# Optimization experiments

Measured on AMD Instinct MI355X. Metric: run time of the kernel, lower is better.

## Reference

```python
import jax, jax.numpy as jnp
import numpy as np

H, C = 4, 32  # heads, per-head channels
EPS = 1e-5


def setup_inputs() -> dict:
    key = jax.random.key(0)
    ks = jax.random.split(key, 12)
    N, E, IN = 100000, 1600000, 16
    lut_idx = jnp.arange(1024, dtype=jnp.int32)
    x = jax.random.normal(ks[0], (N, IN), dtype=jnp.float32)
    # LUT flag column: exactly the lut_idx nodes have value 1.0 (matches x[:,15]==1.0 mask)
    x = x.at[:, 15].set(0.0).at[lut_idx, 15].set(1.0)
    edge_index = jax.random.randint(ks[1], (2, E), 0, N, dtype=jnp.int64)
    s = 0.1
    return {
        "x": x,
        "edge_index": edge_index,
        "lut_idx": lut_idx,
        "W_lin": jax.random.normal(ks[2], (IN, H * C), dtype=jnp.float32) * s,
        "att_src": jax.random.normal(ks[3], (H, C), dtype=jnp.float32) * s,
        "att_dst": jax.random.normal(ks[4], (H, C), dtype=jnp.float32) * s,
        "bias_gat": jnp.zeros((H * C,), dtype=jnp.float32),
        "gamma": jnp.ones((H * C,), dtype=jnp.float32),
        "beta": jnp.zeros((H * C,), dtype=jnp.float32),
        "W1": jax.random.normal(ks[5], (H * C, 32), dtype=jnp.float32) * s,
        "b1": jnp.zeros((32,), dtype=jnp.float32),
        "W2": jax.random.normal(ks[6], (32, 1), dtype=jnp.float32) * s,
        "b2": jnp.zeros((1,), dtype=jnp.float32),
    }


def gat_conv(x, edge_index, W_lin, att_src, att_dst, bias_gat):
    N = x.shape[0]
    # add self-loops (PyG GATConv default)
    loops = jnp.arange(N, dtype=edge_index.dtype)
    src = jnp.concatenate([edge_index[0], loops])
    dst = jnp.concatenate([edge_index[1], loops])
    h = (x @ W_lin).reshape(N, H, C)                      # [N,H,C]
    a_src = (h * att_src[None]).sum(-1)                   # [N,H]
    a_dst = (h * att_dst[None]).sum(-1)                   # [N,H]
    e = jax.nn.leaky_relu(a_src[src] + a_dst[dst], 0.2)   # [Etot,H]
    m = jax.ops.segment_max(e, dst, num_segments=N)       # stable softmax per dst
    e = jnp.exp(e - m[dst])
    denom = jax.ops.segment_sum(e, dst, num_segments=N)
    alpha = e / denom[dst]                                # [Etot,H]
    msg = h[src] * alpha[:, :, None]                      # [Etot,H,C]
    out = jax.ops.segment_sum(msg, dst, num_segments=N)   # [N,H,C]
    return out.reshape(N, H * C) + bias_gat


def reference(x, edge_index, lut_idx, W_lin, att_src, att_dst, bias_gat,
              gamma, beta, W1, b1, W2, b2):
    h = gat_conv(x, edge_index, W_lin, att_src, att_dst, bias_gat)
    # BatchNorm over nodes (training-mode batch stats, biased var, eps=1e-5)
    mean = h.mean(axis=0)
    var = h.var(axis=0)
    h = (h - mean) / jnp.sqrt(var + EPS) * gamma + beta
    h = jax.nn.relu(h)
    emb = h[lut_idx]                                      # masked LUT nodes
    z = jax.nn.leaky_relu(emb @ W1 + b1, 0.01)            # Dropout is identity in eval
    out = z @ W2 + b2                                     # [n_lut, 1]
    return jnp.squeeze(out, axis=0) if out.shape[0] == 1 else out
```

## Files before the change

kernel.cpp:

```cpp
#include <hip/hip_runtime.h>
#include <hip/hip_fp16.h>
#include <cstdint>
#include <cstring>

typedef unsigned int uint;

#define BSHIFT 8
#define NBUCK 512
#define TILE 4096
#define SCAT_T 512
#define FUSE_T 1024
#define SORT_CAP 5120

__device__ __forceinline__ float leaky02(float x) { return x > 0.f ? x : 0.2f * x; }
__device__ __forceinline__ float bflo(uint u) { return __uint_as_float(u << 16); }
__device__ __forceinline__ float bfhi(uint u) { return __uint_as_float(u & 0xffff0000u); }

__device__ __forceinline__ uint pack_bf16x2(float a, float b) {
    uint ua = __float_as_uint(a), ub = __float_as_uint(b);
    ua += 0x7fffu + ((ua >> 16) & 1u);
    ub += 0x7fffu + ((ub >> 16) & 1u);
    return (ua >> 16) | (ub & 0xffff0000u);
}

__device__ __forceinline__ uint packh2(float a, float b) {
    __half ha = __float2half_rn(a), hb = __float2half_rn(b);
    unsigned short ua, ub;
    memcpy(&ua, &ha, 2);
    memcpy(&ub, &hb, 2);
    return (uint)ua | ((uint)ub << 16);
}

__device__ __forceinline__ float h2f_sel(uint2 xw, int head) {
    uint wrd = (head & 2) ? xw.y : xw.x;
    unsigned short us = (unsigned short)((head & 1) ? (wrd >> 16) : (wrd & 0xffffu));
    __half hh; memcpy(&hh, &us, 2);
    return __half2float(hh);
}

__global__ void k_linear(const float* __restrict__ x, const float* __restrict__ W,
                         const float* __restrict__ att_s, const float* __restrict__ att_d,
                         uint* __restrict__ h, float* __restrict__ a_src,
                         float* __restrict__ a_dst, int* __restrict__ cursor,
                         float* __restrict__ sums, float* __restrict__ sumsq, int N) {
    int tid = threadIdx.x;
    __shared__ float sx[32][16];
    __shared__ float sWs[64], sWd[64];
    int j = tid & 63;
    int sub = tid >> 6;
    int n0 = blockIdx.x * 32;

    if (blockIdx.x == 0) {
        cursor[tid] = 0; cursor[tid + 256] = 0;
        if (tid < 128) sums[tid] = 0.f;
        else sumsq[tid - 128] = 0.f;
    }

    float2 wreg[16];
#pragma unroll
    for (int k = 0; k < 16; k++) wreg[k] = ((const float2*)(W + k * 128))[j];

    if (tid < 128) {
        int row = tid >> 2;
        if (n0 + row < N)
            ((float4*)sx)[tid] = ((const float4*)(x + (size_t)n0 * 16))[tid];
    } else if (tid < 192) {
        int t = tid - 128;
        int k = t >> 2, hh = t & 3;
        float s1 = 0.f, s2 = 0.f;
        for (int c = 0; c < 32; c++) {
            float wv = W[k * 128 + hh * 32 + c];
            s1 += wv * att_s[hh * 32 + c];
            s2 += wv * att_d[hh * 32 + c];
        }
        sWs[t] = s1;
        sWd[t] = s2;
    }
    __syncthreads();

#pragma unroll
    for (int i = 0; i < 8; i++) {
        int loc = sub + i * 4;
        int n = n0 + loc;
        if (n >= N) break;
        float acc0 = 0.f, acc1 = 0.f;
#pragma unroll
        for (int k = 0; k < 16; k++) {
            float xk = sx[loc][k];
            acc0 += xk * wreg[k].x;
            acc1 += xk * wreg[k].y;
        }
        h[(size_t)n * 64 + j] = pack_bf16x2(acc0, acc1);
    }

    int loc2 = tid >> 3, hh = (tid >> 1) & 3, sd = tid & 1;
    int n2 = n0 + loc2;
    if (n2 < N) {
        const float* Wm = sd ? sWd : sWs;
        float acc = 0.f;
#pragma unroll
        for (int k = 0; k < 16; k++) acc += sx[loc2][k] * Wm[k * 4 + hh];
        if (sd) a_dst[n2 * 4 + hh] = acc;
        else    a_src[n2 * 4 + hh] = acc;
    }
}

__global__ void kb_scatter(const int* __restrict__ src, const int* __restrict__ dst, int E,
                           int* __restrict__ cursor, uint* __restrict__ pairs) {
    __shared__ int tileCnt[NBUCK], tileCnt2[NBUCK], tileOff[NBUCK], gbase[NBUCK];
    __shared__ int wsum[8], wbase[8];
    __shared__ uint lp[TILE];
    __shared__ unsigned short lb[TILE];
    int tid = threadIdx.x;
    int l = tid & 63, w = tid >> 6;
    int t0 = blockIdx.x * TILE;
    tileCnt[tid] = 0;
    tileCnt2[tid] = 0;
    __syncthreads();
    int dreg[8], sreg[8];
#pragma unroll
    for (int j = 0; j < 8; j++) {
        int idx = t0 + j * SCAT_T + tid;
        if (idx < E) {
            dreg[j] = dst[idx];
            sreg[j] = src[idx];
            atomicAdd(&tileCnt[dreg[j] >> BSHIFT], 1);
        } else dreg[j] = -1;
    }
    __syncthreads();
    int v = tileCnt[tid];
    int s = v;
#pragma unroll
    for (int off = 1; off < 64; off <<= 1) {
        int t = __shfl_up(s, off);
        if (l >= off) s += t;
    }
    if (l == 63) wsum[w] = s;
    __syncthreads();
    if (tid < 8) {
        int b = 0;
        for (int i = 0; i < tid; i++) b += wsum[i];
        wbase[tid] = b;
    }
    __syncthreads();
    int ex = s - v + wbase[w];
    tileOff[tid] = ex;
    if (v > 0) gbase[tid] = atomicAdd(&cursor[tid], v);
    __syncthreads();
#pragma unroll
    for (int j = 0; j < 8; j++) {
        if (dreg[j] >= 0) {
            int bk = dreg[j] >> BSHIFT;
            int r = atomicAdd(&tileCnt2[bk], 1);
            int pos = tileOff[bk] + r;
            lp[pos] = ((uint)sreg[j] << BSHIFT) | (uint)(dreg[j] & 255);
            lb[pos] = (unsigned short)bk;
        }
    }
    __syncthreads();
    int tot = min(TILE, E - t0);
    for (int k = tid; k < tot; k += SCAT_T) {
        int bk = lb[k];
        int lpos = gbase[bk] + (k - tileOff[bk]);
        if (lpos < SORT_CAP)
            pairs[(size_t)bk * SORT_CAP + lpos] = lp[k];
    }
}

__global__ void kb_sortgat(const uint* __restrict__ pairs, const int* __restrict__ cursor,
                           const float* __restrict__ a_src, const float* __restrict__ a_dst,
                           const uint* __restrict__ h, const float* __restrict__ bias,
                           uint* __restrict__ hagg, int N) {
    __shared__ int cnt[256], off0[256], degl[256];
    __shared__ int wsum[4], wbase[4];
    __shared__ uint lcode[SORT_CAP];
    __shared__ uint2 wlds[SORT_CAP];
    __shared__ float4 sad[256], sas[256];
    int tid = threadIdx.x;
    int l = tid & 63, w = tid >> 6;
    int b = blockIdx.x;
    int n0 = b << BSHIFT;
    int nn = min(256, N - n0);
    int ebase = b * SORT_CAP;
    int ecnt = cursor[b];
    if (ecnt > SORT_CAP) ecnt = SORT_CAP;
    if (tid < 256) cnt[tid] = 0;
    if (tid < nn) {
        sad[tid] = ((const float4*)a_dst)[n0 + tid];
        sas[tid] = ((const float4*)a_src)[n0 + tid];
    }
    __syncthreads();
    for (int k = tid; k < ecnt; k += FUSE_T)
        atomicAdd(&cnt[pairs[ebase + k] & 255], 1);
    __syncthreads();
    int v = (tid < 256) ? cnt[tid] : 0;
    int s = v;
#pragma unroll
    for (int off = 1; off < 64; off <<= 1) {
        int t = __shfl_up(s, off);
        if (l >= off) s += t;
    }
    if (tid < 256 && l == 63) wsum[w] = s;
    __syncthreads();
    if (tid < 4) {
        int base = 0;
        for (int i = 0; i < tid; i++) base += wsum[i];
        wbase[tid] = base;
    }
    __syncthreads();
    if (tid < 256) {
        off0[tid] = s - v + wbase[w];
        degl[tid] = v;
    }
    __syncthreads();
    if (tid < 256) cnt[tid] = 0;
    __syncthreads();
    for (int k = tid; k < ecnt; k += FUSE_T) {
        uint p = pairs[ebase + k];
        int ln = p & 255;
        int r = atomicAdd(&cnt[ln], 1);
        lcode[off0[ln] + r] = p;
    }
    __syncthreads();
    for (int k = tid; k < ecnt; k += FUSE_T) {
        uint p = lcode[k];
        int src = (int)(p >> BSHIFT);
        int ln = p & 255;
        float4 as = ((const float4*)a_src)[src];
        float4 ad = sad[ln];
        float w0 = __expf(leaky02(as.x + ad.x));
        float w1 = __expf(leaky02(as.y + ad.y));
        float w2 = __expf(leaky02(as.z + ad.z));
        float w3 = __expf(leaky02(as.w + ad.w));
        wlds[k] = make_uint2(packh2(w0, w1), packh2(w2, w3));
    }
    __syncthreads();
    int q = l >> 4;
    int l16 = l & 15;
    int head = l16 >> 2;
    for (int pass = 0; pass < 4; pass++) {
        int ln = pass * 64 + w * 4 + q;
        if (ln >= nn) continue;
        int d = n0 + ln;
        int ebs = off0[ln];
        int deg = degl[ln];
        float asv = ((const float*)sas)[ln * 4 + head];
        float adv = ((const float*)sad)[ln * 4 + head];
        float wslf = __expf(leaky02(asv + adv));
        uint4 u = ((const uint4*)(h + (size_t)d * 64))[l16];
        float sum = wslf;
        float2 a01 = make_float2(wslf * bflo(u.x), wslf * bfhi(u.x));
        float2 a23 = make_float2(wslf * bflo(u.y), wslf * bfhi(u.y));
        float2 a45 = make_float2(wslf * bflo(u.z), wslf * bfhi(u.z));
        float2 a67 = make_float2(wslf * bflo(u.w), wslf * bfhi(u.w));

        int i = 0;
        for (; i + 3 < deg; i += 4) {
            uint p0 = lcode[ebs + i];
            uint p1 = lcode[ebs + i + 1];
            uint p2 = lcode[ebs + i + 2];
            uint p3 = lcode[ebs + i + 3];
            uint2 x0 = wlds[ebs + i];
            uint2 x1 = wlds[ebs + i + 1];
            uint2 x2 = wlds[ebs + i + 2];
            uint2 x3 = wlds[ebs + i + 3];
            float w0 = h2f_sel(x0, head);
            float w1 = h2f_sel(x1, head);
            float w2 = h2f_sel(x2, head);
            float w3 = h2f_sel(x3, head);
            uint4 u0 = ((const uint4*)(h + (size_t)(p0 >> BSHIFT) * 64))[l16];
            uint4 u1 = ((const uint4*)(h + (size_t)(p1 >> BSHIFT) * 64))[l16];
            uint4 u2 = ((const uint4*)(h + (size_t)(p2 >> BSHIFT) * 64))[l16];
            uint4 u3 = ((const uint4*)(h + (size_t)(p3 >> BSHIFT) * 64))[l16];
            sum += (w0 + w1) + (w2 + w3);
            float2 w02 = {w0, w0}, w12 = {w1, w1}, w22 = {w2, w2}, w32 = {w3, w3};
            a01 += make_float2(bflo(u0.x), bfhi(u0.x)) * w02
                 + make_float2(bflo(u1.x), bfhi(u1.x)) * w12
                 + make_float2(bflo(u2.x), bfhi(u2.x)) * w22
                 + make_float2(bflo(u3.x), bfhi(u3.x)) * w32;
            a23 += make_float2(bflo(u0.y), bfhi(u0.y)) * w02
                 + make_float2(bflo(u1.y), bfhi(u1.y)) * w12
                 + make_float2(bflo(u2.y), bfhi(u2.y)) * w22
                 + make_float2(bflo(u3.y), bfhi(u3.y)) * w32;
            a45 += make_float2(bflo(u0.z), bfhi(u0.z)) * w02
                 + make_float2(bflo(u1.z), bfhi(u1.z)) * w12
                 + make_float2(bflo(u2.z), bfhi(u2.z)) * w22
                 + make_float2(bflo(u3.z), bfhi(u3.z)) * w32;
            a67 += make_float2(bflo(u0.w), bfhi(u0.w)) * w02
                 + make_float2(bflo(u1.w), bfhi(u1.w)) * w12
                 + make_float2(bflo(u2.w), bfhi(u2.w)) * w22
                 + make_float2(bflo(u3.w), bfhi(u3.w)) * w32;
        }
        for (; i < deg; i++) {
            uint p0 = lcode[ebs + i];
            float w0 = h2f_sel(wlds[ebs + i], head);
            uint4 u0 = ((const uint4*)(h + (size_t)(p0 >> BSHIFT) * 64))[l16];
            sum += w0;
            float2 w02 = {w0, w0};
            a01 += make_float2(bflo(u0.x), bfhi(u0.x)) * w02;
            a23 += make_float2(bflo(u0.y), bfhi(u0.y)) * w02;
            a45 += make_float2(bflo(u0.z), bfhi(u0.z)) * w02;
            a67 += make_float2(bflo(u0.w), bfhi(u0.w)) * w02;
        }
        float inv = 1.f / sum;
        float4 b0 = ((const float4*)bias)[2 * l16];
        float4 b1 = ((const float4*)bias)[2 * l16 + 1];
        uint4 o;
        o.x = pack_bf16x2(a01.x * inv + b0.x, a01.y * inv + b0.y);
        o.y = pack_bf16x2(a23.x * inv + b0.z, a23.y * inv + b0.w);
        o.z = pack_bf16x2(a45.x * inv + b1.x, a45.y * inv + b1.y);
        o.w = pack_bf16x2(a67.x * inv + b1.z, a67.y * inv + b1.w);
        ((uint4*)(hagg + (size_t)d * 64))[l16] = o;
    }
}

__global__ void k_bnstats(const uint* __restrict__ hagg, int N,
                          float* __restrict__ sums, float* __restrict__ sumsq) {
    int t = threadIdx.x;
    int cg = t & 31, rs = t >> 5;
    float4 s = make_float4(0.f, 0.f, 0.f, 0.f), q = make_float4(0.f, 0.f, 0.f, 0.f);
    for (int n = blockIdx.x * 8 + rs; n < N; n += gridDim.x * 8) {
        uint2 u = ((const uint2*)(hagg + (size_t)n * 64))[cg];
        float v0 = bflo(u.x), v1 = bfhi(u.x), v2 = bflo(u.y), v3 = bfhi(u.y);
        s.x += v0; s.y += v1; s.z += v2; s.w += v3;
        q.x += v0 * v0; q.y += v1 * v1; q.z += v2 * v2; q.w += v3 * v3;
    }
    __shared__ float4 ls[256], lq[256];
    ls[t] = s; lq[t] = q;
    __syncthreads();
    if (t < 32) {
        float4 S = ls[t], Q = lq[t];
        for (int r = 1; r < 8; r++) {
            float4 a = ls[t + r * 32], b = lq[t + r * 32];
            S.x += a.x; S.y += a.y; S.z += a.z; S.w += a.w;
            Q.x += b.x; Q.y += b.y; Q.z += b.z; Q.w += b.w;
        }
        atomicAdd(&sums[t * 4 + 0], S.x);
        atomicAdd(&sums[t * 4 + 1], S.y);
        atomicAdd(&sums[t * 4 + 2], S.z);
        atomicAdd(&sums[t * 4 + 3], S.w);
        atomicAdd(&sumsq[t * 4 + 0], Q.x);
        atomicAdd(&sumsq[t * 4 + 1], Q.y);
        atomicAdd(&sumsq[t * 4 + 2], Q.z);
        atomicAdd(&sumsq[t * 4 + 3], Q.w);
    }
}

__global__ void k_mlp(const uint* __restrict__ hagg, const int* __restrict__ lut,
                      const float* __restrict__ sums, const float* __restrict__ sumsq,
                      const float* __restrict__ gamma, const float* __restrict__ beta,
                      const float* __restrict__ W1, const float* __restrict__ b1,
                      const float* __restrict__ W2, const float* __restrict__ b2,
                      float* __restrict__ out, int N, int nlut) {
    int blk = blockIdx.x;
    if (blk >= nlut) return;
    int node = lut[blk];
    int lane = threadIdx.x;
    __shared__ float v[128];
    float invN = 1.f / (float)N;
    uint u = hagg[(size_t)node * 64 + lane];
    int c0 = 2 * lane, c1 = 2 * lane + 1;
    {
        float mean = sums[c0] * invN;
        float var = sumsq[c0] * invN - mean * mean;
        float val = (bflo(u) - mean) / sqrtf(var + 1e-5f) * gamma[c0] + beta[c0];
        v[c0] = fmaxf(val, 0.f);
        mean = sums[c1] * invN;
        var = sumsq[c1] * invN - mean * mean;
        val = (bfhi(u) - mean) / sqrtf(var + 1e-5f) * gamma[c1] + beta[c1];
        v[c1] = fmaxf(val, 0.f);
    }
    __syncthreads();
    float r = 0.f;
    if (lane < 32) {
        float z = b1[lane];
        for (int c = 0; c < 128; c++) z += v[c] * W1[c * 32 + lane];
        z = z > 0.f ? z : 0.01f * z;
        r = z * W2[lane];
    }
#pragma unroll
    for (int off = 16; off >= 1; off >>= 1) r += __shfl_xor(r, off);
    if (lane == 0) out[blk] = r + b2[0];
}

extern "C" void kernel_launch(void* const* d_in, const int* in_sizes, int n_in,
                              void* d_out, int out_size, void* d_ws, size_t ws_size,
                              hipStream_t stream) {
    const float* x     = (const float*)d_in[0];
    const int*   edges = (const int*)d_in[1];
    const int*   lut   = (const int*)d_in[2];
    const float* W_lin = (const float*)d_in[3];
    const float* att_s = (const float*)d_in[4];
    const float* att_d = (const float*)d_in[5];
    const float* bias  = (const float*)d_in[6];
    const float* gamma = (const float*)d_in[7];
    const float* beta  = (const float*)d_in[8];
    const float* W1    = (const float*)d_in[9];
    const float* b1    = (const float*)d_in[10];
    const float* W2    = (const float*)d_in[11];
    const float* b2    = (const float*)d_in[12];

    int N = in_sizes[0] / 16;
    int E = in_sizes[1] / 2;
    int nlut = in_sizes[2];
    int B = (N + 255) >> BSHIFT;

    const int* esrc = edges;
    const int* edst = edges + E;

    char* ws = (char*)d_ws;
    size_t off = 0;
    auto alloc = [&](size_t bytes) -> void* {
        void* p = ws + off;
        off += (bytes + 255) & ~(size_t)255;
        return p;
    };
    uint*  h       = (uint*)alloc((size_t)N * 64 * 4);
    uint*  hagg    = (uint*)alloc((size_t)N * 64 * 4);
    float* a_src   = (float*)alloc((size_t)N * 4 * 4);
    float* a_dst   = (float*)alloc((size_t)N * 4 * 4);
    uint*  pairs   = (uint*)alloc((size_t)B * SORT_CAP * 4);
    int*   cursor  = (int*)alloc((size_t)NBUCK * 4);
    float* sums    = (float*)alloc(128 * 4);
    float* sumsq   = (float*)alloc(128 * 4);

    k_linear<<<(N + 31) / 32, 256, 0, stream>>>(x, W_lin, att_s, att_d, h,
                                                a_src, a_dst, cursor, sums, sumsq, N);
    kb_scatter<<<(E + TILE - 1) / TILE, SCAT_T, 0, stream>>>(esrc, edst, E, cursor, pairs);
    kb_sortgat<<<B, FUSE_T, 0, stream>>>(pairs, cursor, a_src, a_dst, h, bias, hagg, N);
    k_bnstats<<<256, 256, 0, stream>>>(hagg, N, sums, sumsq);
    k_mlp<<<nlut, 64, 0, stream>>>(hagg, lut, sums, sumsq, gamma, beta, W1, b1, W2, b2,
                                   (float*)d_out, N, nlut);
}
```

Measured before the change: 233.9 us.

## Fuse BatchNorm statistics into GAT aggregation and write only LUT rows

Removes the separate k_bnstats kernel. Per-channel sum and sum-of-squares are now accumulated in registers inside kb_sortgat, reduced with shuffles and LDS, and added to global sums with atomics. Aggregated rows are written to hagg only for LUT nodes, marked by a flag array that k_linear clears and kb_scatter sets. This skips most of the hagg write and the full re-read, at the cost of more per-block atomics and extra reduction work. The counting-sort scatter pass and the attention-weight pass are also merged, lcode now stores raw source indices, and a launch-bounds hint is added.

Result: faster. 211.3 us (-9.7%).

```diff
diff --git a/kernel.cpp b/kernel.cpp
--- a/kernel.cpp
+++ b/kernel.cpp
@@ -42,7 +42,8 @@
                          const float* __restrict__ att_s, const float* __restrict__ att_d,
                          uint* __restrict__ h, float* __restrict__ a_src,
                          float* __restrict__ a_dst, int* __restrict__ cursor,
-                         float* __restrict__ sums, float* __restrict__ sumsq, int N) {
+                         float* __restrict__ sums, float* __restrict__ sumsq,
+                         unsigned char* __restrict__ flags, int N) {
     int tid = threadIdx.x;
     __shared__ float sx[32][16];
     __shared__ float sWs[64], sWd[64];
@@ -55,6 +56,7 @@
         if (tid < 128) sums[tid] = 0.f;
         else sumsq[tid - 128] = 0.f;
     }
+    if (tid < 32 && n0 + tid < N) flags[n0 + tid] = 0;
 
     float2 wreg[16];
 #pragma unroll
@@ -106,7 +108,9 @@
 }
 
 __global__ void kb_scatter(const int* __restrict__ src, const int* __restrict__ dst, int E,
-                           int* __restrict__ cursor, uint* __restrict__ pairs) {
+                           int* __restrict__ cursor, uint* __restrict__ pairs,
+                           const int* __restrict__ lut, int nlut,
+                           unsigned char* __restrict__ flags) {
     __shared__ int tileCnt[NBUCK], tileCnt2[NBUCK], tileOff[NBUCK], gbase[NBUCK];
     __shared__ int wsum[8], wbase[8];
     __shared__ uint lp[TILE];
@@ -114,6 +118,9 @@
     int tid = threadIdx.x;
     int l = tid & 63, w = tid >> 6;
     int t0 = blockIdx.x * TILE;
+    if (blockIdx.x == 0) {
+        for (int k = tid; k < nlut; k += SCAT_T) flags[lut[k]] = 1;
+    }
     tileCnt[tid] = 0;
     tileCnt2[tid] = 0;
     __syncthreads();
@@ -167,15 +174,18 @@
     }
 }
 
-__global__ void kb_sortgat(const uint* __restrict__ pairs, const int* __restrict__ cursor,
+__global__ void __launch_bounds__(1024, 8) kb_sortgat(
+                           const uint* __restrict__ pairs, const int* __restrict__ cursor,
                            const float* __restrict__ a_src, const float* __restrict__ a_dst,
                            const uint* __restrict__ h, const float* __restrict__ bias,
-                           uint* __restrict__ hagg, int N) {
+                           const unsigned char* __restrict__ flags,
+                           uint* __restrict__ hagg,
+                           float* __restrict__ sums, float* __restrict__ sumsq, int N) {
     __shared__ int cnt[256], off0[256], degl[256];
     __shared__ int wsum[4], wbase[4];
     __shared__ uint lcode[SORT_CAP];
     __shared__ uint2 wlds[SORT_CAP];
-    __shared__ float4 sad[256], sas[256];
+    __shared__ float4 sad[256];
     int tid = threadIdx.x;
     int l = tid & 63, w = tid >> 6;
     int b = blockIdx.x;
@@ -185,10 +195,7 @@
     int ecnt = cursor[b];
     if (ecnt > SORT_CAP) ecnt = SORT_CAP;
     if (tid < 256) cnt[tid] = 0;
-    if (tid < nn) {
-        sad[tid] = ((const float4*)a_dst)[n0 + tid];
-        sas[tid] = ((const float4*)a_src)[n0 + tid];
-    }
+    if (tid < nn) sad[tid] = ((const float4*)a_dst)[n0 + tid];
     __syncthreads();
     for (int k = tid; k < ecnt; k += FUSE_T)
         atomicAdd(&cnt[pairs[ebase + k] & 255], 1);
@@ -218,33 +225,32 @@
     for (int k = tid; k < ecnt; k += FUSE_T) {
         uint p = pairs[ebase + k];
         int ln = p & 255;
+        int src = (int)(p >> BSHIFT);
         int r = atomicAdd(&cnt[ln], 1);
-        lcode[off0[ln] + r] = p;
-    }
-    __syncthreads();
-    for (int k = tid; k < ecnt; k += FUSE_T) {
-        uint p = lcode[k];
-        int src = (int)(p >> BSHIFT);
-        int ln = p & 255;
+        int pos = off0[ln] + r;
+        lcode[pos] = (uint)src;
         float4 as = ((const float4*)a_src)[src];
         float4 ad = sad[ln];
-        float w0 = __expf(leaky02(as.x + ad.x));
-        float w1 = __expf(leaky02(as.y + ad.y));
-        float w2 = __expf(leaky02(as.z + ad.z));
-        float w3 = __expf(leaky02(as.w + ad.w));
-        wlds[k] = make_uint2(packh2(w0, w1), packh2(w2, w3));
+        wlds[pos] = make_uint2(
+            packh2(__expf(leaky02(as.x + ad.x)), __expf(leaky02(as.y + ad.y))),
+            packh2(__expf(leaky02(as.z + ad.z)), __expf(leaky02(as.w + ad.w))));
     }
     __syncthreads();
     int q = l >> 4;
     int l16 = l & 15;
     int head = l16 >> 2;
+    float4 b0 = ((const float4*)bias)[2 * l16];
+    float4 b1 = ((const float4*)bias)[2 * l16 + 1];
+    float sv[8], sq[8];
+#pragma unroll
+    for (int j = 0; j < 8; j++) { sv[j] = 0.f; sq[j] = 0.f; }
     for (int pass = 0; pass < 4; pass++) {
         int ln = pass * 64 + w * 4 + q;
         if (ln >= nn) continue;
         int d = n0 + ln;
         int ebs = off0[ln];
         int deg = degl[ln];
-        float asv = ((const float*)sas)[ln * 4 + head];
+        float asv = a_src[d * 4 + head];
         float adv = ((const float*)sad)[ln * 4 + head];
         float wslf = __expf(leaky02(asv + adv));
         uint4 u = ((const uint4*)(h + (size_t)d * 64))[l16];
@@ -268,10 +274,10 @@
             float w1 = h2f_sel(x1, head);
             float w2 = h2f_sel(x2, head);
             float w3 = h2f_sel(x3, head);
-            uint4 u0 = ((const uint4*)(h + (size_t)(p0 >> BSHIFT) * 64))[l16];
-            uint4 u1 = ((const uint4*)(h + (size_t)(p1 >> BSHIFT) * 64))[l16];
-            uint4 u2 = ((const uint4*)(h + (size_t)(p2 >> BSHIFT) * 64))[l16];
-            uint4 u3 = ((const uint4*)(h + (size_t)(p3 >> BSHIFT) * 64))[l16];
+            uint4 u0 = ((const uint4*)(h + (size_t)p0 * 64))[l16];
+            uint4 u1 = ((const uint4*)(h + (size_t)p1 * 64))[l16];
+            uint4 u2 = ((const uint4*)(h + (size_t)p2 * 64))[l16];
+            uint4 u3 = ((const uint4*)(h + (size_t)p3 * 64))[l16];
             sum += (w0 + w1) + (w2 + w3);
             float2 w02 = {w0, w0}, w12 = {w1, w1}, w22 = {w2, w2}, w32 = {w3, w3};
             a01 += make_float2(bflo(u0.x), bfhi(u0.x)) * w02
@@ -294,7 +300,7 @@
         for (; i < deg; i++) {
             uint p0 = lcode[ebs + i];
             float w0 = h2f_sel(wlds[ebs + i], head);
-            uint4 u0 = ((const uint4*)(h + (size_t)(p0 >> BSHIFT) * 64))[l16];
+            uint4 u0 = ((const uint4*)(h + (size_t)p0 * 64))[l16];
             sum += w0;
             float2 w02 = {w0, w0};
             a01 += make_float2(bflo(u0.x), bfhi(u0.x)) * w02;
@@ -303,46 +309,55 @@
             a67 += make_float2(bflo(u0.w), bfhi(u0.w)) * w02;
         }
         float inv = 1.f / sum;
-        float4 b0 = ((const float4*)bias)[2 * l16];
-        float4 b1 = ((const float4*)bias)[2 * l16 + 1];
-        uint4 o;
-        o.x = pack_bf16x2(a01.x * inv + b0.x, a01.y * inv + b0.y);
-        o.y = pack_bf16x2(a23.x * inv + b0.z, a23.y * inv + b0.w);
-        o.z = pack_bf16x2(a45.x * inv + b1.x, a45.y * inv + b1.y);
-        o.w = pack_bf16x2(a67.x * inv + b1.z, a67.y * inv + b1.w);
-        ((uint4*)(hagg + (size_t)d * 64))[l16] = o;
-    }
-}
-
-__global__ void k_bnstats(const uint* __restrict__ hagg, int N,
-                          float* __restrict__ sums, float* __restrict__ sumsq) {
-    int t = threadIdx.x;
-    int cg = t & 31, rs = t >> 5;
-    float4 s = make_float4(0.f, 0.f, 0.f, 0.f), q = make_float4(0.f, 0.f, 0.f, 0.f);
-    for (int n = blockIdx.x * 8 + rs; n < N; n += gridDim.x * 8) {
-        uint2 u = ((const uint2*)(hagg + (size_t)n * 64))[cg];
-        float v0 = bflo(u.x), v1 = bfhi(u.x), v2 = bflo(u.y), v3 = bfhi(u.y);
-        s.x += v0; s.y += v1; s.z += v2; s.w += v3;
-        q.x += v0 * v0; q.y += v1 * v1; q.z += v2 * v2; q.w += v3 * v3;
-    }
-    __shared__ float4 ls[256], lq[256];
-    ls[t] = s; lq[t] = q;
-    __syncthreads();
-    if (t < 32) {
-        float4 S = ls[t], Q = lq[t];
-        for (int r = 1; r < 8; r++) {
-            float4 a = ls[t + r * 32], b = lq[t + r * 32];
-            S.x += a.x; S.y += a.y; S.z += a.z; S.w += a.w;
-            Q.x += b.x; Q.y += b.y; Q.z += b.z; Q.w += b.w;
-        }
-        atomicAdd(&sums[t * 4 + 0], S.x);
-        atomicAdd(&sums[t * 4 + 1], S.y);
-        atomicAdd(&sums[t * 4 + 2], S.z);
-        atomicAdd(&sums[t * 4 + 3], S.w);
-        atomicAdd(&sumsq[t * 4 + 0], Q.x);
-        atomicAdd(&sumsq[t * 4 + 1], Q.y);
-        atomicAdd(&sumsq[t * 4 + 2], Q.z);
-        atomicAdd(&sumsq[t * 4 + 3], Q.w);
+        float v0 = a01.x * inv + b0.x;
+        float v1 = a01.y * inv + b0.y;
+        float v2 = a23.x * inv + b0.z;
+        float v3 = a23.y * inv + b0.w;
+        float v4 = a45.x * inv + b1.x;
+        float v5 = a45.y * inv + b1.y;
+        float v6 = a67.x * inv + b1.z;
+        float v7 = a67.y * inv + b1.w;
+        sv[0] += v0; sq[0] += v0 * v0;
+        sv[1] += v1; sq[1] += v1 * v1;
+        sv[2] += v2; sq[2] += v2 * v2;
+        sv[3] += v3; sq[3] += v3 * v3;
+        sv[4] += v4; sq[4] += v4 * v4;
+        sv[5] += v5; sq[5] += v5 * v5;
+        sv[6] += v6; sq[6] += v6 * v6;
+        sv[7] += v7; sq[7] += v7 * v7;
+        if (flags[d]) {
+            uint4 o;
+            o.x = pack_bf16x2(v0, v1);
+            o.y = pack_bf16x2(v2, v3);
+            o.z = pack_bf16x2(v4, v5);
+            o.w = pack_bf16x2(v6, v7);
+            ((uint4*)(hagg + (size_t)d * 64))[l16] = o;
+        }
+    }
+    __syncthreads();
+#pragma unroll
+    for (int j = 0; j < 8; j++) {
+        sv[j] += __shfl_xor(sv[j], 16);
+        sv[j] += __shfl_xor(sv[j], 32);
+        sq[j] += __shfl_xor(sq[j], 16);
+        sq[j] += __shfl_xor(sq[j], 32);
+    }
+    float* red = (float*)lcode;
+    if (l < 16) {
+#pragma unroll
+        for (int j = 0; j < 8; j++) {
+            red[(w * 16 + l) * 16 + j] = sv[j];
+            red[(w * 16 + l) * 16 + 8 + j] = sq[j];
+        }
+    }
+    __syncthreads();
+    if (tid < 256) {
+        int lg = tid >> 4, j = tid & 15;
+        float tot = 0.f;
+#pragma unroll
+        for (int ww = 0; ww < 16; ww++) tot += red[(ww * 16 + lg) * 16 + j];
+        if (j < 8) atomicAdd(&sums[lg * 8 + j], tot);
+        else       atomicAdd(&sumsq[lg * 8 + j - 8], tot);
     }
 }
 
@@ -423,12 +438,15 @@
     int*   cursor  = (int*)alloc((size_t)NBUCK * 4);
     float* sums    = (float*)alloc(128 * 4);
     float* sumsq   = (float*)alloc(128 * 4);
+    unsigned char* flags = (unsigned char*)alloc((size_t)N);
 
     k_linear<<<(N + 31) / 32, 256, 0, stream>>>(x, W_lin, att_s, att_d, h,
-                                                a_src, a_dst, cursor, sums, sumsq, N);
-    kb_scatter<<<(E + TILE - 1) / TILE, SCAT_T, 0, stream>>>(esrc, edst, E, cursor, pairs);
-    kb_sortgat<<<B, FUSE_T, 0, stream>>>(pairs, cursor, a_src, a_dst, h, bias, hagg, N);
-    k_bnstats<<<256, 256, 0, stream>>>(hagg, N, sums, sumsq);
+                                                a_src, a_dst, cursor, sums, sumsq,
+                                                flags, N);
+    kb_scatter<<<(E + TILE - 1) / TILE, SCAT_T, 0, stream>>>(esrc, edst, E, cursor, pairs,
+                                                             lut, nlut, flags);
+    kb_sortgat<<<B, FUSE_T, 0, stream>>>(pairs, cursor, a_src, a_dst, h, bias,
+                                         flags, hagg, sums, sumsq, N);
     k_mlp<<<nlut, 64, 0, stream>>>(hagg, lut, sums, sumsq, gamma, beta, W1, b1, W2, b2,
                                    (float*)d_out, N, nlut);
 }
```
